# Kernel tuning notes

Measured on AMD Instinct MI355X. Metric: run time of the kernel, lower is better.

Reference implementation:

```python
import jax, jax.numpy as jnp
import numpy as np

NKV = 8      # n_head_kv
G = 8        # n_head // n_head_kv
D = 64       # head_dim (hardcoded in source views)
NH = NKV * G # n_head = 64


def rotate_half(x):
    x1, x2 = x[..., : D // 2], x[..., D // 2:]
    return jnp.concatenate((-x2, x1), axis=-1)


def setup_inputs() -> dict:
    key = jax.random.key(0)
    ks = jax.random.split(key, 9)
    B, S, H = 2, 1024, 4096
    hidden_states = jax.random.normal(ks[0], (B, S, H), dtype=jnp.float32)
    alibi = jnp.zeros((B * NH, 1, S), dtype=jnp.float32)            # unused in this forward path
    attention_mask = jnp.zeros((B, 1, S, S), dtype=jnp.float32)      # unused (is_causal=True)
    cos = jax.random.uniform(ks[1], (S, D), dtype=jnp.float32, minval=-1.0, maxval=1.0)
    sin = jax.random.uniform(ks[2], (S, D), dtype=jnp.float32, minval=-1.0, maxval=1.0)
    wq = jax.random.normal(ks[3], (H, H), dtype=jnp.float32) * 0.02          # Linear weight (out, in)
    wk = jax.random.normal(ks[4], (NKV * D, H), dtype=jnp.float32) * 0.02
    wv = jax.random.normal(ks[5], (NKV * D, H), dtype=jnp.float32) * 0.02
    wd = jax.random.normal(ks[6], (H, H), dtype=jnp.float32) * 0.02          # dense weight
    return {"hidden_states": hidden_states, "alibi": alibi, "attention_mask": attention_mask,
            "cos": cos, "sin": sin, "wq": wq, "wk": wk, "wv": wv, "wd": wd}


def reference(hidden_states, alibi, attention_mask, cos, sin, wq, wk, wv, wd):
    B, S, H = hidden_states.shape
    # fused-style projections (Linear: x @ W.T, no bias)
    # q: [B, S, NKV, G, D] -> [B, NKV, G, S, D]; head h = kv_group*G + j (group-major, matches source rearrange)
    q = (hidden_states @ wq.T).reshape(B, S, NKV, G, D).transpose(0, 2, 3, 1, 4)
    k = (hidden_states @ wk.T).reshape(B, S, NKV, D).transpose(0, 2, 1, 3)   # [B, NKV, S, D]
    v = (hidden_states @ wv.T).reshape(B, S, NKV, D).transpose(0, 2, 1, 3)
    # RoPE (cos/sin broadcast over batch/head dims)
    q = q * cos + rotate_half(q) * sin
    k = k * cos + rotate_half(k) * sin
    # grouped-query attention without materializing broadcast K/V
    inv_norm = jnp.asarray(1.0 / np.sqrt(D), dtype=hidden_states.dtype)
    scores = jnp.einsum('bkgsd,bktd->bkgst', q, k) * inv_norm        # [B, NKV, G, S, S]
    causal = jnp.tril(jnp.ones((S, S), dtype=bool))
    neg = jnp.finfo(scores.dtype).min
    scores = jnp.where(causal, scores, scores + neg)
    probs = jax.nn.softmax(scores, axis=-1)
    out = jnp.einsum('bkgst,bktd->bkgsd', probs, v)                  # [B, NKV, G, S, D]
    out = out.reshape(B, NH, S, D).transpose(0, 2, 1, 3).reshape(B, S, NH * D)
    return out @ wd.T
```

## Files before the change

### kernel.cpp

```cpp
#include <hip/hip_runtime.h>
#include <hip/hip_bf16.h>
#include <cstdint>

typedef short short8 __attribute__((ext_vector_type(8)));
typedef __bf16 bf16x8 __attribute__((ext_vector_type(8)));
typedef float float4v __attribute__((ext_vector_type(4)));
typedef float float16v __attribute__((ext_vector_type(16)));

#define NKV 8
#define G 8
#define D 64
#define NH 64
#define BB 2
#define S 1024
#define H 4096
#define MROWS (BB*S)
#define NQKV (H + 2*NKV*D)

__device__ __forceinline__ unsigned short f2b(float f) {
    union { float f; uint32_t u; } v; v.f = f;
    uint32_t u = v.u;
    uint32_t r = (u + 0x7FFFu + ((u >> 16) & 1u)) >> 16;
    return (unsigned short)r;
}
__device__ __forceinline__ float b2f(unsigned short b) {
    union { float f; uint32_t u; } v; v.u = ((uint32_t)b) << 16;
    return v.f;
}

__device__ __forceinline__ void gload_lds16(const unsigned short* g, unsigned short* l) {
    __builtin_amdgcn_global_load_lds(
        (const __attribute__((address_space(1))) uint32_t*)g,
        (__attribute__((address_space(3))) uint32_t*)l, 16, 0, 0);
}

__global__ void cvt_all(const float* __restrict__ hs, const float* __restrict__ wq,
                        const float* __restrict__ wk, const float* __restrict__ wv,
                        const float* __restrict__ wd,
                        unsigned short* __restrict__ hs_b, unsigned short* __restrict__ wqkv_b,
                        unsigned short* __restrict__ wd_b) {
    const size_t N0 = (size_t)MROWS * H;
    const size_t N1 = (size_t)H * H;
    const size_t N2 = (size_t)512 * H;
    const size_t N3 = (size_t)512 * H;
    const size_t N4 = (size_t)H * H;
    const size_t total4 = (N0 + N1 + N2 + N3 + N4) / 4;
    size_t i = (size_t)blockIdx.x * blockDim.x + threadIdx.x;
    const size_t stride = (size_t)gridDim.x * blockDim.x;
    for (; i < total4; i += stride) {
        size_t e = i * 4;
        const float* s; unsigned short* d;
        if (e < N0)                { s = hs + e;                  d = hs_b + e; }
        else if (e < N0+N1)        { s = wq + (e-N0);             d = wqkv_b + (e-N0); }
        else if (e < N0+N1+N2)     { s = wk + (e-N0-N1);          d = wqkv_b + N1 + (e-N0-N1); }
        else if (e < N0+N1+N2+N3)  { s = wv + (e-N0-N1-N2);       d = wqkv_b + N1+N2 + (e-N0-N1-N2); }
        else                       { s = wd + (e-N0-N1-N2-N3);    d = wd_b + (e-N0-N1-N2-N3); }
        float4 f = *(const float4*)s;
        ushort4 o;
        o.x = f2b(f.x); o.y = f2b(f.y); o.z = f2b(f.z); o.w = f2b(f.w);
        *(ushort4*)d = o;
    }
}

template <bool BF16_OUT>
__global__ __launch_bounds__(256) void gemm_nt(
    const unsigned short* __restrict__ A, const unsigned short* __restrict__ W,
    void* __restrict__ Cv, int M, int N, int K) {
    __shared__ unsigned short As[128 * 32];
    __shared__ unsigned short Bs[128 * 32];
    const int bm = blockIdx.y * 128, bn = blockIdx.x * 128;
    const int tid = threadIdx.x;
    const int w = tid >> 6, lane = tid & 63;
    const int n32 = lane & 31, khalf = lane >> 5;
    const int wm = (w & 1) * 64, wn = (w >> 1) * 64;

    const int r0 = tid >> 2;
    const int c0 = (tid & 3) ^ ((r0 >> 2) & 3);
    const unsigned short* pA0 = A + (size_t)(bm + r0) * K + c0 * 8;
    const unsigned short* pA1 = A + (size_t)(bm + r0 + 64) * K + c0 * 8;
    const unsigned short* pW0 = W + (size_t)(bn + r0) * K + c0 * 8;
    const unsigned short* pW1 = W + (size_t)(bn + r0 + 64) * K + c0 * 8;
    unsigned short* Asl0 = As + tid * 8;
    unsigned short* Asl1 = As + 2048 + tid * 8;
    unsigned short* Bsl0 = Bs + tid * 8;
    unsigned short* Bsl1 = Bs + 2048 + tid * 8;

    const unsigned short* aP[2][2];
    const unsigned short* bP[2][2];
#pragma unroll
    for (int g = 0; g < 2; g++)
#pragma unroll
        for (int s = 0; s < 2; s++) {
            int cp = ((s << 1) | khalf) ^ ((n32 >> 2) & 3);
            aP[g][s] = &As[(wm + g * 32 + n32) * 32 + cp * 8];
            bP[g][s] = &Bs[(wn + g * 32 + n32) * 32 + cp * 8];
        }

    float16v acc[2][2] = {};

    const int iters = K >> 5;
    for (int it = 0; it < iters; ++it) {
        __syncthreads();
        gload_lds16(pA0, Asl0);
        gload_lds16(pA1, Asl1);
        gload_lds16(pW0, Bsl0);
        gload_lds16(pW1, Bsl1);
        pA0 += 32; pA1 += 32; pW0 += 32; pW1 += 32;
        __syncthreads();
        bf16x8 af[2][2], bf[2][2];
#pragma unroll
        for (int g = 0; g < 2; g++)
#pragma unroll
            for (int s = 0; s < 2; s++) {
                af[g][s] = *(const bf16x8*)aP[g][s];
                bf[g][s] = *(const bf16x8*)bP[g][s];
            }
#pragma unroll
        for (int s = 0; s < 2; s++)
#pragma unroll
            for (int mg = 0; mg < 2; mg++)
#pragma unroll
                for (int ng = 0; ng < 2; ng++)
                    acc[mg][ng] = __builtin_amdgcn_mfma_f32_32x32x16_bf16(
                        af[mg][s], bf[ng][s], acc[mg][ng], 0, 0, 0);
    }

#pragma unroll
    for (int mg = 0; mg < 2; mg++) {
#pragma unroll
        for (int ng = 0; ng < 2; ng++) {
            int gcol = bn + wn + ng * 32 + n32;
#pragma unroll
            for (int reg = 0; reg < 16; reg++) {
                int grow = bm + wm + mg * 32 + (reg & 3) + 8 * (reg >> 2) + 4 * khalf;
                if (BF16_OUT)
                    ((unsigned short*)Cv)[(size_t)grow * N + gcol] = f2b(acc[mg][ng][reg]);
                else
                    ((float*)Cv)[(size_t)grow * N + gcol] = acc[mg][ng][reg];
            }
        }
    }
}

__global__ void rope_scatter(const unsigned short* __restrict__ qkv,
                             const float* __restrict__ cosb, const float* __restrict__ sinb,
                             unsigned short* __restrict__ qa, unsigned short* __restrict__ ka,
                             unsigned short* __restrict__ vt) {
    int idx = blockIdx.x * blockDim.x + threadIdx.x;
    const int total = MROWS * NQKV;
    const int stride = gridDim.x * blockDim.x;
    for (; idx < total; idx += stride) {
        int row = idx / NQKV, o = idx - row * NQKV;
        int b = row >> 10, s = row & 1023;
        float x = b2f(qkv[idx]);
        if (o < H) {
            int kv = o >> 9, g = (o >> 6) & 7, d = o & 63;
            int po = (d < 32) ? idx + 32 : idx - 32;
            float partner = b2f(qkv[po]);
            float rot = (d < 32) ? -partner : partner;
            float y = x * cosb[s * 64 + d] + rot * sinb[s * 64 + d];
            int h = b * 64 + kv * 8 + g;
            qa[(size_t)h * (S * D) + s * 64 + d] = f2b(y);
        } else if (o < H + 512) {
            int o2 = o - H;
            int kv = o2 >> 6, d = o2 & 63;
            int po = (d < 32) ? idx + 32 : idx - 32;
            float partner = b2f(qkv[po]);
            float rot = (d < 32) ? -partner : partner;
            float y = x * cosb[s * 64 + d] + rot * sinb[s * 64 + d];
            ka[(size_t)(b * NKV + kv) * (S * D) + s * 64 + d] = f2b(y);
        } else {
            int o2 = o - H - 512;
            int kv = o2 >> 6, d = o2 & 63;
            vt[(size_t)(b * NKV + kv) * (D * S) + (size_t)d * S + s] = qkv[idx];
        }
    }
}

__global__ __launch_bounds__(256) void attn_kernel(
    const unsigned short* __restrict__ qa, const unsigned short* __restrict__ ka,
    const unsigned short* __restrict__ vt, unsigned short* __restrict__ out) {
    __shared__ unsigned short Ks[64 * 72];
    __shared__ unsigned short Vs[64 * 72];
    __shared__ unsigned short Ps[4 * 16 * 72];
    const int p = blockIdx.x;
    const int yy = blockIdx.y;
    const int b = yy >> 5, kvh = (yy >> 2) & 7, gp = yy & 3;
    const int h0 = b * 64 + kvh * 8 + gp * 2;
    const int tid = threadIdx.x, w = tid >> 6, lane = tid & 63;
    const int col = lane & 15, quad = lane >> 4;
    const unsigned short* Kg = ka + (size_t)(b * NKV + kvh) * (S * D);
    const unsigned short* Vg = vt + (size_t)(b * NKV + kvh) * (D * S);
    const int srow = tid >> 3, scc = (tid & 7) * 8;
    float4v zero4 = {0.f, 0.f, 0.f, 0.f};
    const float SC2 = 0.125f * 1.44269504089f;

#pragma unroll
    for (int part = 0; part < 2; part++) {
        const int qt = part ? (15 - p) : p;
        const int qb = qt * 64;

        bf16x8 aq[2][2];
#pragma unroll
        for (int hd = 0; hd < 2; hd++)
#pragma unroll
            for (int c = 0; c < 2; c++)
                aq[hd][c] = *(const bf16x8*)&qa[(size_t)(h0 + hd) * (S * D) + (size_t)qb * D
                                               + (w * 16 + col) * 64 + c * 32 + quad * 8];

        float m_run[2][4], l_run[2][4];
        float4v o_acc[2][4];
#pragma unroll
        for (int hd = 0; hd < 2; hd++) {
#pragma unroll
            for (int r = 0; r < 4; r++) { m_run[hd][r] = -1e30f; l_run[hd][r] = 0.f; }
#pragma unroll
            for (int dg = 0; dg < 4; dg++) o_acc[hd][dg] = zero4;
        }

        for (int kt = 0; kt <= qt; kt++) {
            const int kb = kt * 64;
            __syncthreads();
            *(short8*)&Ks[srow * 72 + scc]        = *(const short8*)&Kg[(kb + srow) * 64 + scc];
            *(short8*)&Ks[(srow + 32) * 72 + scc] = *(const short8*)&Kg[(kb + srow + 32) * 64 + scc];
            *(short8*)&Vs[srow * 72 + scc]        = *(const short8*)&Vg[(size_t)srow * S + kb + scc];
            *(short8*)&Vs[(srow + 32) * 72 + scc] = *(const short8*)&Vg[(size_t)(srow + 32) * S + kb + scc];
            __syncthreads();

#pragma unroll
            for (int hd = 0; hd < 2; hd++) {
                float4v sc[4];
#pragma unroll
                for (int n16 = 0; n16 < 4; n16++) {
                    bf16x8 bk0 = *(const bf16x8*)&Ks[(n16 * 16 + col) * 72 + quad * 8];
                    bf16x8 bk1 = *(const bf16x8*)&Ks[(n16 * 16 + col) * 72 + 32 + quad * 8];
                    float4v a = __builtin_amdgcn_mfma_f32_16x16x32_bf16(aq[hd][0], bk0, zero4, 0, 0, 0);
                    sc[n16] = __builtin_amdgcn_mfma_f32_16x16x32_bf16(aq[hd][1], bk1, a, 0, 0, 0);
                }
#pragma unroll
                for (int n16 = 0; n16 < 4; n16++) {
                    int key = kb + n16 * 16 + col;
#pragma unroll
                    for (int r = 0; r < 4; r++) {
                        int qrow = qb + w * 16 + quad * 4 + r;
                        float sv = sc[n16][r] * SC2;
                        sc[n16][r] = (key <= qrow) ? sv : -1e30f;
                    }
                }
#pragma unroll
                for (int r = 0; r < 4; r++) {
                    float mx = fmaxf(fmaxf(sc[0][r], sc[1][r]), fmaxf(sc[2][r], sc[3][r]));
#pragma unroll
                    for (int off = 1; off < 16; off <<= 1) mx = fmaxf(mx, __shfl_xor(mx, off));
                    float mnew = fmaxf(m_run[hd][r], mx);
                    float alpha = __builtin_amdgcn_exp2f(m_run[hd][r] - mnew);
                    float rsum = 0.f;
#pragma unroll
                    for (int n16 = 0; n16 < 4; n16++) {
                        float pr = __builtin_amdgcn_exp2f(sc[n16][r] - mnew);
                        sc[n16][r] = pr;
                        rsum += pr;
                    }
#pragma unroll
                    for (int off = 1; off < 16; off <<= 1) rsum += __shfl_xor(rsum, off);
                    l_run[hd][r] = l_run[hd][r] * alpha + rsum;
                    m_run[hd][r] = mnew;
#pragma unroll
                    for (int dg = 0; dg < 4; dg++) o_acc[hd][dg][r] *= alpha;
                }
#pragma unroll
                for (int n16 = 0; n16 < 4; n16++)
#pragma unroll
                    for (int r = 0; r < 4; r++)
                        Ps[w * 1152 + (quad * 4 + r) * 72 + n16 * 16 + col] = f2b(sc[n16][r]);
                bf16x8 ap[2];
#pragma unroll
                for (int c = 0; c < 2; c++)
                    ap[c] = *(const bf16x8*)&Ps[w * 1152 + col * 72 + c * 32 + quad * 8];
#pragma unroll
                for (int dg = 0; dg < 4; dg++) {
                    bf16x8 bv0 = *(const bf16x8*)&Vs[(dg * 16 + col) * 72 + quad * 8];
                    bf16x8 bv1 = *(const bf16x8*)&Vs[(dg * 16 + col) * 72 + 32 + quad * 8];
                    float4v t = __builtin_amdgcn_mfma_f32_16x16x32_bf16(ap[0], bv0, o_acc[hd][dg], 0, 0, 0);
                    o_acc[hd][dg] = __builtin_amdgcn_mfma_f32_16x16x32_bf16(ap[1], bv1, t, 0, 0, 0);
                }
            }
        }
#pragma unroll
        for (int hd = 0; hd < 2; hd++) {
            const int hcol = ((h0 + hd) & 63) * 64;
#pragma unroll
            for (int r = 0; r < 4; r++) {
                float inv = 1.f / l_run[hd][r];
                int grow = b * S + qb + w * 16 + quad * 4 + r;
#pragma unroll
                for (int dg = 0; dg < 4; dg++)
                    out[(size_t)grow * H + hcol + dg * 16 + col] = f2b(o_acc[hd][dg][r] * inv);
            }
        }
    }
}

extern "C" void kernel_launch(void* const* d_in, const int* in_sizes, int n_in,
                              void* d_out, int out_size, void* d_ws, size_t ws_size,
                              hipStream_t stream) {
    const float* hs   = (const float*)d_in[0];
    const float* cosb = (const float*)d_in[3];
    const float* sinb = (const float*)d_in[4];
    const float* wq   = (const float*)d_in[5];
    const float* wk   = (const float*)d_in[6];
    const float* wv   = (const float*)d_in[7];
    const float* wd   = (const float*)d_in[8];

    char* p = (char*)d_ws;
    auto alloc = [&](size_t bytes) { char* r = p; p += (bytes + 255) & ~(size_t)255; return r; };
    unsigned short* wqkv_b = (unsigned short*)alloc((size_t)NQKV * H * 2);
    unsigned short* wd_b   = (unsigned short*)alloc((size_t)H * H * 2);
    unsigned short* qkv    = (unsigned short*)alloc((size_t)MROWS * NQKV * 2);
    unsigned short* qa     = (unsigned short*)alloc((size_t)BB * NH * S * D * 2);
    unsigned short* ka     = (unsigned short*)alloc((size_t)BB * NKV * S * D * 2);
    unsigned short* vt     = (unsigned short*)alloc((size_t)BB * NKV * S * D * 2);
    unsigned short* hs_b   = (unsigned short*)alloc((size_t)MROWS * H * 2);
    unsigned short* ao     = hs_b;

    cvt_all<<<4096, 256, 0, stream>>>(hs, wq, wk, wv, wd, hs_b, wqkv_b, wd_b);

    gemm_nt<true><<<dim3(NQKV / 128, MROWS / 128), 256, 0, stream>>>(hs_b, wqkv_b, qkv, MROWS, NQKV, H);
    rope_scatter<<<4096, 256, 0, stream>>>(qkv, cosb, sinb, qa, ka, vt);
    attn_kernel<<<dim3(8, 64), 256, 0, stream>>>(qa, ka, vt, ao);
    gemm_nt<false><<<dim3(H / 128, MROWS / 128), 256, 0, stream>>>(ao, wd_b, d_out, MROWS, H, H);
}
```

Baseline: 514.3 us.

## Fuse RoPE and scatter into QKV GEMM epilogue; retile attention with 32x32 MFMA

The RoPE/scatter pass moves into the QKV GEMM epilogue, so the intermediate qkv buffer and the separate kernel that rereads it go away. The attention kernel is also restructured. Each block now handles one head and a 128-row query tile, using 32x32x16 MFMAs with 32 rows per wave in place of two heads with 16x16 tiles. Fully masked key tiles are skipped per wave. The tradeoffs are more registers in attention, strided V-transpose stores in the GEMM epilogue, and a new causal-skip scheme that must still cover the diagonal correctly.

Measured after the change: 586.8 us. 1.14x slower.

```diff
diff --git a/kernel.cpp b/kernel.cpp
--- a/kernel.cpp
+++ b/kernel.cpp
@@ -62,10 +62,12 @@
     }
 }
 
-template <bool BF16_OUT>
-__global__ __launch_bounds__(256) void gemm_nt(
+__global__ __launch_bounds__(256) void gemm_qkv(
     const unsigned short* __restrict__ A, const unsigned short* __restrict__ W,
-    void* __restrict__ Cv, int M, int N, int K) {
+    const float* __restrict__ cosb, const float* __restrict__ sinb,
+    unsigned short* __restrict__ qa, unsigned short* __restrict__ ka,
+    unsigned short* __restrict__ vt) {
+    const int K = H;
     __shared__ unsigned short As[128 * 32];
     __shared__ unsigned short Bs[128 * 32];
     const int bm = blockIdx.y * 128, bn = blockIdx.x * 128;
@@ -97,7 +99,6 @@
         }
 
     float16v acc[2][2] = {};
-
     const int iters = K >> 5;
     for (int it = 0; it < iters; ++it) {
         __syncthreads();
@@ -125,56 +126,126 @@
                         af[mg][s], bf[ng][s], acc[mg][ng], 0, 0, 0);
     }
 
-#pragma unroll
-    for (int mg = 0; mg < 2; mg++) {
+    const int base = bn + wn;
+    if (base < H) {
+        const int hloc = base >> 6;
+#pragma unroll
+        for (int mg = 0; mg < 2; mg++) {
+#pragma unroll
+            for (int reg = 0; reg < 16; reg++) {
+                int grow = bm + wm + mg * 32 + (reg & 3) + 8 * (reg >> 2) + 4 * khalf;
+                int s = grow & 1023, b = grow >> 10;
+                float c0 = cosb[s * 64 + n32],      s0 = sinb[s * 64 + n32];
+                float c1 = cosb[s * 64 + 32 + n32], s1 = sinb[s * 64 + 32 + n32];
+                float x0 = acc[mg][0][reg], x1 = acc[mg][1][reg];
+                size_t off = ((size_t)(b * 64 + hloc) * S + s) * 64;
+                qa[off + n32]      = f2b(x0 * c0 - x1 * s0);
+                qa[off + 32 + n32] = f2b(x1 * c1 + x0 * s1);
+            }
+        }
+    } else if (base < H + 512) {
+        const int kvh = (base - H) >> 6;
+#pragma unroll
+        for (int mg = 0; mg < 2; mg++) {
+#pragma unroll
+            for (int reg = 0; reg < 16; reg++) {
+                int grow = bm + wm + mg * 32 + (reg & 3) + 8 * (reg >> 2) + 4 * khalf;
+                int s = grow & 1023, b = grow >> 10;
+                float c0 = cosb[s * 64 + n32],      s0 = sinb[s * 64 + n32];
+                float c1 = cosb[s * 64 + 32 + n32], s1 = sinb[s * 64 + 32 + n32];
+                float x0 = acc[mg][0][reg], x1 = acc[mg][1][reg];
+                size_t off = ((size_t)(b * NKV + kvh) * S + s) * 64;
+                ka[off + n32]      = f2b(x0 * c0 - x1 * s0);
+                ka[off + 32 + n32] = f2b(x1 * c1 + x0 * s1);
+            }
+        }
+    } else {
+        const int kvh = (base - H - 512) >> 6;
+#pragma unroll
+        for (int mg = 0; mg < 2; mg++) {
+#pragma unroll
+            for (int reg = 0; reg < 16; reg++) {
+                int grow = bm + wm + mg * 32 + (reg & 3) + 8 * (reg >> 2) + 4 * khalf;
+                int s = grow & 1023, b = grow >> 10;
+                size_t hb = (size_t)(b * NKV + kvh) * 64;
+                vt[(hb + n32) * S + s]      = f2b(acc[mg][0][reg]);
+                vt[(hb + 32 + n32) * S + s] = f2b(acc[mg][1][reg]);
+            }
+        }
+    }
+}
+
+__global__ __launch_bounds__(256) void gemm_nt_f32(
+    const unsigned short* __restrict__ A, const unsigned short* __restrict__ W,
+    float* __restrict__ C, int M, int N, int K) {
+    __shared__ unsigned short As[128 * 32];
+    __shared__ unsigned short Bs[128 * 32];
+    const int bm = blockIdx.y * 128, bn = blockIdx.x * 128;
+    const int tid = threadIdx.x;
+    const int w = tid >> 6, lane = tid & 63;
+    const int n32 = lane & 31, khalf = lane >> 5;
+    const int wm = (w & 1) * 64, wn = (w >> 1) * 64;
+
+    const int r0 = tid >> 2;
+    const int c0 = (tid & 3) ^ ((r0 >> 2) & 3);
+    const unsigned short* pA0 = A + (size_t)(bm + r0) * K + c0 * 8;
+    const unsigned short* pA1 = A + (size_t)(bm + r0 + 64) * K + c0 * 8;
+    const unsigned short* pW0 = W + (size_t)(bn + r0) * K + c0 * 8;
+    const unsigned short* pW1 = W + (size_t)(bn + r0 + 64) * K + c0 * 8;
+    unsigned short* Asl0 = As + tid * 8;
+    unsigned short* Asl1 = As + 2048 + tid * 8;
+    unsigned short* Bsl0 = Bs + tid * 8;
+    unsigned short* Bsl1 = Bs + 2048 + tid * 8;
+
+    const unsigned short* aP[2][2];
+    const unsigned short* bP[2][2];
+#pragma unroll
+    for (int g = 0; g < 2; g++)
+#pragma unroll
+        for (int s = 0; s < 2; s++) {
+            int cp = ((s << 1) | khalf) ^ ((n32 >> 2) & 3);
+            aP[g][s] = &As[(wm + g * 32 + n32) * 32 + cp * 8];
+            bP[g][s] = &Bs[(wn + g * 32 + n32) * 32 + cp * 8];
+        }
+
+    float16v acc[2][2] = {};
+    const int iters = K >> 5;
+    for (int it = 0; it < iters; ++it) {
+        __syncthreads();
+        gload_lds16(pA0, Asl0);
+        gload_lds16(pA1, Asl1);
+        gload_lds16(pW0, Bsl0);
+        gload_lds16(pW1, Bsl1);
+        pA0 += 32; pA1 += 32; pW0 += 32; pW1 += 32;
+        __syncthreads();
+        bf16x8 af[2][2], bf[2][2];
+#pragma unroll
+        for (int g = 0; g < 2; g++)
+#pragma unroll
+            for (int s = 0; s < 2; s++) {
+                af[g][s] = *(const bf16x8*)aP[g][s];
+                bf[g][s] = *(const bf16x8*)bP[g][s];
+            }
+#pragma unroll
+        for (int s = 0; s < 2; s++)
+#pragma unroll
+            for (int mg = 0; mg < 2; mg++)
+#pragma unroll
+                for (int ng = 0; ng < 2; ng++)
+                    acc[mg][ng] = __builtin_amdgcn_mfma_f32_32x32x16_bf16(
+                        af[mg][s], bf[ng][s], acc[mg][ng], 0, 0, 0);
+    }
+#pragma unroll
+    for (int mg = 0; mg < 2; mg++)
 #pragma unroll
         for (int ng = 0; ng < 2; ng++) {
             int gcol = bn + wn + ng * 32 + n32;
 #pragma unroll
             for (int reg = 0; reg < 16; reg++) {
                 int grow = bm + wm + mg * 32 + (reg & 3) + 8 * (reg >> 2) + 4 * khalf;
-                if (BF16_OUT)
-                    ((unsigned short*)Cv)[(size_t)grow * N + gcol] = f2b(acc[mg][ng][reg]);
-                else
-                    ((float*)Cv)[(size_t)grow * N + gcol] = acc[mg][ng][reg];
-            }
-        }
-    }
-}
-
-__global__ void rope_scatter(const unsigned short* __restrict__ qkv,
-                             const float* __restrict__ cosb, const float* __restrict__ sinb,
-                             unsigned short* __restrict__ qa, unsigned short* __restrict__ ka,
-                             unsigned short* __restrict__ vt) {
-    int idx = blockIdx.x * blockDim.x + threadIdx.x;
-    const int total = MROWS * NQKV;
-    const int stride = gridDim.x * blockDim.x;
-    for (; idx < total; idx += stride) {
-        int row = idx / NQKV, o = idx - row * NQKV;
-        int b = row >> 10, s = row & 1023;
-        float x = b2f(qkv[idx]);
-        if (o < H) {
-            int kv = o >> 9, g = (o >> 6) & 7, d = o & 63;
-            int po = (d < 32) ? idx + 32 : idx - 32;
-            float partner = b2f(qkv[po]);
-            float rot = (d < 32) ? -partner : partner;
-            float y = x * cosb[s * 64 + d] + rot * sinb[s * 64 + d];
-            int h = b * 64 + kv * 8 + g;
-            qa[(size_t)h * (S * D) + s * 64 + d] = f2b(y);
-        } else if (o < H + 512) {
-            int o2 = o - H;
-            int kv = o2 >> 6, d = o2 & 63;
-            int po = (d < 32) ? idx + 32 : idx - 32;
-            float partner = b2f(qkv[po]);
-            float rot = (d < 32) ? -partner : partner;
-            float y = x * cosb[s * 64 + d] + rot * sinb[s * 64 + d];
-            ka[(size_t)(b * NKV + kv) * (S * D) + s * 64 + d] = f2b(y);
-        } else {
-            int o2 = o - H - 512;
-            int kv = o2 >> 6, d = o2 & 63;
-            vt[(size_t)(b * NKV + kv) * (D * S) + (size_t)d * S + s] = qkv[idx];
-        }
-    }
+                C[(size_t)grow * N + gcol] = acc[mg][ng][reg];
+            }
+        }
 }
 
 __global__ __launch_bounds__(256) void attn_kernel(
@@ -182,43 +253,37 @@
     const unsigned short* __restrict__ vt, unsigned short* __restrict__ out) {
     __shared__ unsigned short Ks[64 * 72];
     __shared__ unsigned short Vs[64 * 72];
-    __shared__ unsigned short Ps[4 * 16 * 72];
+    __shared__ unsigned short Ps[4 * 32 * 72];
     const int p = blockIdx.x;
-    const int yy = blockIdx.y;
-    const int b = yy >> 5, kvh = (yy >> 2) & 7, gp = yy & 3;
-    const int h0 = b * 64 + kvh * 8 + gp * 2;
+    const int h = blockIdx.y;
+    const int b = h >> 6, kvh = (h >> 3) & 7;
     const int tid = threadIdx.x, w = tid >> 6, lane = tid & 63;
-    const int col = lane & 15, quad = lane >> 4;
+    const int n32 = lane & 31, khalf = lane >> 5;
     const unsigned short* Kg = ka + (size_t)(b * NKV + kvh) * (S * D);
     const unsigned short* Vg = vt + (size_t)(b * NKV + kvh) * (D * S);
     const int srow = tid >> 3, scc = (tid & 7) * 8;
-    float4v zero4 = {0.f, 0.f, 0.f, 0.f};
     const float SC2 = 0.125f * 1.44269504089f;
+    unsigned short* Pw = Ps + w * 32 * 72;
 
 #pragma unroll
     for (int part = 0; part < 2; part++) {
-        const int qt = part ? (15 - p) : p;
-        const int qb = qt * 64;
-
-        bf16x8 aq[2][2];
-#pragma unroll
-        for (int hd = 0; hd < 2; hd++)
-#pragma unroll
-            for (int c = 0; c < 2; c++)
-                aq[hd][c] = *(const bf16x8*)&qa[(size_t)(h0 + hd) * (S * D) + (size_t)qb * D
-                                               + (w * 16 + col) * 64 + c * 32 + quad * 8];
-
-        float m_run[2][4], l_run[2][4];
-        float4v o_acc[2][4];
-#pragma unroll
-        for (int hd = 0; hd < 2; hd++) {
-#pragma unroll
-            for (int r = 0; r < 4; r++) { m_run[hd][r] = -1e30f; l_run[hd][r] = 0.f; }
-#pragma unroll
-            for (int dg = 0; dg < 4; dg++) o_acc[hd][dg] = zero4;
-        }
-
-        for (int kt = 0; kt <= qt; kt++) {
+        const int qt = part ? (7 - p) : p;
+        const int qb = qt * 128;
+        const int wbase = qb + w * 32;
+
+        bf16x8 aq[4];
+#pragma unroll
+        for (int kst = 0; kst < 4; kst++)
+            aq[kst] = *(const bf16x8*)&qa[(size_t)h * (S * D)
+                                          + (size_t)(wbase + n32) * 64 + kst * 16 + khalf * 8];
+
+        float m_run[16], l_run[16];
+        float16v o_acc[2] = {};
+#pragma unroll
+        for (int r = 0; r < 16; r++) { m_run[r] = -1e30f; l_run[r] = 0.f; }
+
+        const int nkt = 2 * qt + 2;
+        for (int kt = 0; kt < nkt; kt++) {
             const int kb = kt * 64;
             __syncthreads();
             *(short8*)&Ks[srow * 72 + scc]        = *(const short8*)&Kg[(kb + srow) * 64 + scc];
@@ -226,77 +291,60 @@
             *(short8*)&Vs[srow * 72 + scc]        = *(const short8*)&Vg[(size_t)srow * S + kb + scc];
             *(short8*)&Vs[(srow + 32) * 72 + scc] = *(const short8*)&Vg[(size_t)(srow + 32) * S + kb + scc];
             __syncthreads();
-
-#pragma unroll
-            for (int hd = 0; hd < 2; hd++) {
-                float4v sc[4];
-#pragma unroll
-                for (int n16 = 0; n16 < 4; n16++) {
-                    bf16x8 bk0 = *(const bf16x8*)&Ks[(n16 * 16 + col) * 72 + quad * 8];
-                    bf16x8 bk1 = *(const bf16x8*)&Ks[(n16 * 16 + col) * 72 + 32 + quad * 8];
-                    float4v a = __builtin_amdgcn_mfma_f32_16x16x32_bf16(aq[hd][0], bk0, zero4, 0, 0, 0);
-                    sc[n16] = __builtin_amdgcn_mfma_f32_16x16x32_bf16(aq[hd][1], bk1, a, 0, 0, 0);
+            if (kb > wbase) continue;
+
+            float16v sacc[2] = {};
+#pragma unroll
+            for (int kst = 0; kst < 4; kst++) {
+                bf16x8 bk0 = *(const bf16x8*)&Ks[n32 * 72 + kst * 16 + khalf * 8];
+                bf16x8 bk1 = *(const bf16x8*)&Ks[(32 + n32) * 72 + kst * 16 + khalf * 8];
+                sacc[0] = __builtin_amdgcn_mfma_f32_32x32x16_bf16(aq[kst], bk0, sacc[0], 0, 0, 0);
+                sacc[1] = __builtin_amdgcn_mfma_f32_32x32x16_bf16(aq[kst], bk1, sacc[1], 0, 0, 0);
+            }
+            const bool domask = (kb + 63 > wbase);
+#pragma unroll
+            for (int r = 0; r < 16; r++) {
+                float s0 = sacc[0][r] * SC2, s1 = sacc[1][r] * SC2;
+                int prow = (r & 3) + 8 * (r >> 2) + 4 * khalf;
+                if (domask) {
+                    int qrow = wbase + prow;
+                    if (kb + n32 > qrow)      s0 = -1e30f;
+                    if (kb + 32 + n32 > qrow) s1 = -1e30f;
                 }
-#pragma unroll
-                for (int n16 = 0; n16 < 4; n16++) {
-                    int key = kb + n16 * 16 + col;
-#pragma unroll
-                    for (int r = 0; r < 4; r++) {
-                        int qrow = qb + w * 16 + quad * 4 + r;
-                        float sv = sc[n16][r] * SC2;
-                        sc[n16][r] = (key <= qrow) ? sv : -1e30f;
-                    }
-                }
-#pragma unroll
-                for (int r = 0; r < 4; r++) {
-                    float mx = fmaxf(fmaxf(sc[0][r], sc[1][r]), fmaxf(sc[2][r], sc[3][r]));
-#pragma unroll
-                    for (int off = 1; off < 16; off <<= 1) mx = fmaxf(mx, __shfl_xor(mx, off));
-                    float mnew = fmaxf(m_run[hd][r], mx);
-                    float alpha = __builtin_amdgcn_exp2f(m_run[hd][r] - mnew);
-                    float rsum = 0.f;
-#pragma unroll
-                    for (int n16 = 0; n16 < 4; n16++) {
-                        float pr = __builtin_amdgcn_exp2f(sc[n16][r] - mnew);
-                        sc[n16][r] = pr;
-                        rsum += pr;
-                    }
-#pragma unroll
-                    for (int off = 1; off < 16; off <<= 1) rsum += __shfl_xor(rsum, off);
-                    l_run[hd][r] = l_run[hd][r] * alpha + rsum;
-                    m_run[hd][r] = mnew;
-#pragma unroll
-                    for (int dg = 0; dg < 4; dg++) o_acc[hd][dg][r] *= alpha;
-                }
-#pragma unroll
-                for (int n16 = 0; n16 < 4; n16++)
-#pragma unroll
-                    for (int r = 0; r < 4; r++)
-                        Ps[w * 1152 + (quad * 4 + r) * 72 + n16 * 16 + col] = f2b(sc[n16][r]);
-                bf16x8 ap[2];
-#pragma unroll
-                for (int c = 0; c < 2; c++)
-                    ap[c] = *(const bf16x8*)&Ps[w * 1152 + col * 72 + c * 32 + quad * 8];
-#pragma unroll
-                for (int dg = 0; dg < 4; dg++) {
-                    bf16x8 bv0 = *(const bf16x8*)&Vs[(dg * 16 + col) * 72 + quad * 8];
-                    bf16x8 bv1 = *(const bf16x8*)&Vs[(dg * 16 + col) * 72 + 32 + quad * 8];
-                    float4v t = __builtin_amdgcn_mfma_f32_16x16x32_bf16(ap[0], bv0, o_acc[hd][dg], 0, 0, 0);
-                    o_acc[hd][dg] = __builtin_amdgcn_mfma_f32_16x16x32_bf16(ap[1], bv1, t, 0, 0, 0);
-                }
-            }
-        }
-#pragma unroll
-        for (int hd = 0; hd < 2; hd++) {
-            const int hcol = ((h0 + hd) & 63) * 64;
-#pragma unroll
-            for (int r = 0; r < 4; r++) {
-                float inv = 1.f / l_run[hd][r];
-                int grow = b * S + qb + w * 16 + quad * 4 + r;
-#pragma unroll
-                for (int dg = 0; dg < 4; dg++)
-                    out[(size_t)grow * H + hcol + dg * 16 + col] = f2b(o_acc[hd][dg][r] * inv);
-            }
+                float mx = fmaxf(s0, s1);
+#pragma unroll
+                for (int off = 1; off < 32; off <<= 1) mx = fmaxf(mx, __shfl_xor(mx, off));
+                float mnew = fmaxf(m_run[r], mx);
+                float alpha = __builtin_amdgcn_exp2f(m_run[r] - mnew);
+                float p0 = __builtin_amdgcn_exp2f(s0 - mnew);
+                float p1 = __builtin_amdgcn_exp2f(s1 - mnew);
+                float rsum = p0 + p1;
+#pragma unroll
+                for (int off = 1; off < 32; off <<= 1) rsum += __shfl_xor(rsum, off);
+                m_run[r] = mnew;
+                l_run[r] = l_run[r] * alpha + rsum;
+                o_acc[0][r] *= alpha;
+                o_acc[1][r] *= alpha;
+                Pw[prow * 72 + n32]      = f2b(p0);
+                Pw[prow * 72 + 32 + n32] = f2b(p1);
+            }
+#pragma unroll
+            for (int kst = 0; kst < 4; kst++) {
+                bf16x8 ap  = *(const bf16x8*)&Pw[n32 * 72 + kst * 16 + khalf * 8];
+                bf16x8 bv0 = *(const bf16x8*)&Vs[n32 * 72 + kst * 16 + khalf * 8];
+                bf16x8 bv1 = *(const bf16x8*)&Vs[(32 + n32) * 72 + kst * 16 + khalf * 8];
+                o_acc[0] = __builtin_amdgcn_mfma_f32_32x32x16_bf16(ap, bv0, o_acc[0], 0, 0, 0);
+                o_acc[1] = __builtin_amdgcn_mfma_f32_32x32x16_bf16(ap, bv1, o_acc[1], 0, 0, 0);
+            }
+        }
+        const size_t hcol = (size_t)(h & 63) * 64;
+#pragma unroll
+        for (int r = 0; r < 16; r++) {
+            float inv = 1.f / l_run[r];
+            int grow = b * S + wbase + (r & 3) + 8 * (r >> 2) + 4 * khalf;
+            size_t off = (size_t)grow * H + hcol;
+            out[off + n32]      = f2b(o_acc[0][r] * inv);
+            out[off + 32 + n32] = f2b(o_acc[1][r] * inv);
         }
     }
 }
@@ -316,7 +364,6 @@
     auto alloc = [&](size_t bytes) { char* r = p; p += (bytes + 255) & ~(size_t)255; return r; };
     unsigned short* wqkv_b = (unsigned short*)alloc((size_t)NQKV * H * 2);
     unsigned short* wd_b   = (unsigned short*)alloc((size_t)H * H * 2);
-    unsigned short* qkv    = (unsigned short*)alloc((size_t)MROWS * NQKV * 2);
     unsigned short* qa     = (unsigned short*)alloc((size_t)BB * NH * S * D * 2);
     unsigned short* ka     = (unsigned short*)alloc((size_t)BB * NKV * S * D * 2);
     unsigned short* vt     = (unsigned short*)alloc((size_t)BB * NKV * S * D * 2);
@@ -324,9 +371,7 @@
     unsigned short* ao     = hs_b;
 
     cvt_all<<<4096, 256, 0, stream>>>(hs, wq, wk, wv, wd, hs_b, wqkv_b, wd_b);
-
-    gemm_nt<true><<<dim3(NQKV / 128, MROWS / 128), 256, 0, stream>>>(hs_b, wqkv_b, qkv, MROWS, NQKV, H);
-    rope_scatter<<<4096, 256, 0, stream>>>(qkv, cosb, sinb, qa, ka, vt);
-    attn_kernel<<<dim3(8, 64), 256, 0, stream>>>(qa, ka, vt, ao);
-    gemm_nt<false><<<dim3(H / 128, MROWS / 128), 256, 0, stream>>>(ao, wd_b, d_out, MROWS, H, H);
-}
+    gemm_qkv<<<dim3(NQKV / 128, MROWS / 128), 256, 0, stream>>>(hs_b, wqkv_b, cosb, sinb, qa, ka, vt);
+    attn_kernel<<<dim3(4, 128), 256, 0, stream>>>(qa, ka, vt, ao);
+    gemm_nt_f32<<<dim3(H / 128, MROWS / 128), 256, 0, stream>>>(ao, wd_b, (float*)d_out, MROWS, H, H);
+}
```
